# Performance work log

Measured on AMD Instinct MI355X. Metric: run time of the kernel, lower is better.

Reference implementation:

```python
import jax, jax.numpy as jnp
import numpy as np
from jax import lax

# sym8 analysis low-pass filter (pywt.Wavelet('sym8').dec_lo, matches MATLAB Lo_D)
FL = 16
DEC_LO = np.array([-0.0033824159510061256, -0.0005421323317911481, 0.03169508781149298,
                   0.007607487324917605, -0.1432942383508097, -0.061273359067658524,
                   0.4813596512583722, 0.7771857517005235, 0.3644418948353314,
                   -0.051945838107709037, -0.027219029917056003, 0.049137179673607506,
                   0.003808752013890615, -0.01495225833704823, -0.0003029205147213668,
                   0.0018899503327594609])
REC_LO = DEC_LO[::-1]
REC_HI = ((-1.0) ** np.arange(FL)) * DEC_LO  # qmf: rec_hi[k] = (-1)^k * rec_lo[FL-1-k]
DEC_HI = REC_HI[::-1]
# lax.conv does correlation, np.convolve flips -> store flipped filters
_DEC_K = jnp.asarray(np.stack([DEC_LO[::-1], DEC_HI[::-1]])[:, None, :], dtype=jnp.float32)  # (2,1,16)
_REC_K = jnp.asarray(np.stack([REC_LO[::-1], REC_HI[::-1]])[None, :, :], dtype=jnp.float32)  # (1,2,16)
DN = ('NCH', 'OIH', 'NCH')


def _dwt(x):
    # single-level pywt dwt, mode='symmetric': pad FL-1 each side, full conv, take odd indices
    B, C, S = x.shape
    xe = jnp.pad(x.reshape(B * C, 1, S), ((0, 0), (0, 0), (FL - 1, FL - 1)), mode='symmetric')[..., 1:]
    y = lax.conv_general_dilated(xe, _DEC_K, (2,), 'VALID', dimension_numbers=DN)
    L = y.shape[-1]  # floor((S + FL - 1)/2)
    y = y.reshape(B, C, 2, L)
    return y[:, :, 0], y[:, :, 1]


def _idwt(a, d):
    # single-level pywt idwt: upsample (len 2L-1), full conv, trim FL-2 each side
    B, C, L = a.shape
    c = jnp.stack([a, d], axis=2).reshape(B * C, 2, L)
    y = lax.conv_general_dilated(c, _REC_K, (1,), [(1, 1)], lhs_dilation=(2,), dimension_numbers=DN)
    return y.reshape(B, C, y.shape[-1])  # length 2L - FL + 2


def _wavedec(x, level):
    ds = []
    a = x
    for _ in range(level):
        a, d = _dwt(a)
        ds.append(d)
    return a, ds[::-1]  # coarsest first, matching pywt [cA_n, cD_n, ..., cD_1]


def _waverec(a, ds):
    for d in ds:
        if a.shape[-1] == d.shape[-1] + 1:  # static shapes -> Python if is jit-safe
            a = a[..., :-1]
        a = _idwt(a, d)
    return a


def _c1(x, w, b):
    # 1x1 conv: w (O,C), x (B,C,L)
    return jnp.einsum('oc,bcl->bol', w, x) + b[:, None]


def _inorm(x, eps=1e-5):
    m = jnp.mean(x, axis=-1, keepdims=True)
    v = jnp.mean((x - m) ** 2, axis=-1, keepdims=True)
    return (x - m) * lax.rsqrt(v + eps)


def _block(x, w_w, w_b, ca_w, ca_b, cd_w, cd_b, m1_w, m1_b, m2_w, m2_b):
    xn = _inorm(x)
    xs = lax.conv_general_dilated(xn, w_w, (1,), [(1, 1)], dimension_numbers=DN) + w_b[:, None]
    level = cd_w.shape[0]
    a, ds = _wavedec(xn, level)
    a = _c1(a, ca_w, ca_b)
    ds = [_c1(d, cd_w[i], cd_b[i]) for i, d in enumerate(ds)]
    xw = _waverec(a, ds)[..., : xs.shape[-1]]
    xo = x + jax.nn.gelu(xw + xs, approximate=False)
    xon = _inorm(xo)
    h = jax.nn.gelu(_c1(xon, m1_w, m1_b), approximate=False)
    return xo + _c1(h, m2_w, m2_b)


def _forward(x, lift_w, lift_b, blk_w_w, blk_w_b, blk_ca_w, blk_ca_b, blk_cd_w, blk_cd_b,
             blk_m1_w, blk_m1_b, blk_m2_w, blk_m2_b, p1_w, p1_b, p2_w, p2_b):
    B, S = x.shape
    grid = jnp.broadcast_to(jnp.linspace(-1.0, 1.0, S, dtype=x.dtype)[None, None, :], (B, 1, S))
    h = jnp.concatenate([x[:, None, :], grid], axis=1)  # (B, 2, S)
    h = _c1(h, lift_w, lift_b)
    for i in range(blk_w_w.shape[0]):
        h = _block(h, blk_w_w[i], blk_w_b[i], blk_ca_w[i], blk_ca_b[i], blk_cd_w[i],
                   blk_cd_b[i], blk_m1_w[i], blk_m1_b[i], blk_m2_w[i], blk_m2_b[i])
    h = jax.nn.gelu(_c1(h, p1_w, p1_b), approximate=False)
    return _c1(h, p2_w, p2_b)


def setup_inputs():
    key = jax.random.key(0)
    ks = jax.random.split(key, 17)
    B, S, C, NB, LV = 16, 8192, 64, 4, 4
    H = 2 * C  # mlp_expansion=2
    f = jnp.float32
    rn = lambda k, shape, s: jax.random.normal(k, shape, dtype=f) * s
    return {
        'x': jax.random.normal(ks[0], (B, S), dtype=f),
        'lift_w': rn(ks[1], (C, 2), 0.5), 'lift_b': rn(ks[2], (C,), 0.05),
        'blk_w_w': rn(ks[3], (NB, C, C, 3), 0.07), 'blk_w_b': rn(ks[4], (NB, C), 0.05),
        'blk_ca_w': rn(ks[5], (NB, C, C), 0.12), 'blk_ca_b': rn(ks[6], (NB, C), 0.05),
        'blk_cd_w': rn(ks[7], (NB, LV, C, C), 0.12), 'blk_cd_b': rn(ks[8], (NB, LV, C), 0.05),
        'blk_m1_w': rn(ks[9], (NB, H, C), 0.12), 'blk_m1_b': rn(ks[10], (NB, H), 0.05),
        'blk_m2_w': rn(ks[11], (NB, C, H), 0.08), 'blk_m2_b': rn(ks[12], (NB, C), 0.05),
        'p1_w': rn(ks[13], (C // 2, C), 0.12), 'p1_b': rn(ks[14], (C // 2,), 0.05),
        'p2_w': rn(ks[15], (C, C // 2), 0.17), 'p2_b': rn(ks[16], (C,), 0.05),
    }


def reference(x, lift_w, lift_b, blk_w_w, blk_w_b, blk_ca_w, blk_ca_b, blk_cd_w, blk_cd_b,
              blk_m1_w, blk_m1_b, blk_m2_w, blk_m2_b, p1_w, p1_b, p2_w, p2_b):
    return _forward(x, lift_w, lift_b, blk_w_w, blk_w_b, blk_ca_w, blk_ca_b, blk_cd_w,
                    blk_cd_b, blk_m1_w, blk_m1_b, blk_m2_w, blk_m2_b, p1_w, p1_b, p2_w, p2_b)
```

## Files before the change

### kernel.cpp

```cpp
#include <hip/hip_runtime.h>
#include <math.h>

#define S_LEN 8192
#define B_N   16
#define NBC   1024
#define L1v 4103
#define L2v 2059
#define L3v 1037
#define L4v 526
#define LP1 4104
#define LP2 2060
#define LP3 1040
#define LP4 528

#define OFF_CONV 0
#define OFF_M1   49152
#define OFF_M2   81920
#define OFF_CD   114688
#define OFF_CA   180224
#define OFF_P1   196608
#define OFF_P2   198656
#define WTOT     200704

typedef __attribute__((ext_vector_type(8))) short bf16x8;
typedef __attribute__((ext_vector_type(4))) float f32x4;

__constant__ float c_dlo[16] = {
    -0.0033824159510061256f, -0.0005421323317911481f,  0.03169508781149298f,
     0.007607487324917605f,  -0.1432942383508097f,    -0.061273359067658524f,
     0.4813596512583722f,     0.7771857517005235f,     0.3644418948353314f,
    -0.05194583810770904f,   -0.027219029917056003f,   0.049137179673607506f,
     0.003808752013890615f,  -0.01495225833704823f,   -0.0003029205147213668f,
     0.0018899503327594609f
};
__constant__ float c_dhi[16] = {
    -0.0018899503327594609f, -0.0003029205147213668f,  0.01495225833704823f,
     0.003808752013890615f,  -0.049137179673607506f,  -0.027219029917056003f,
     0.05194583810770904f,    0.3644418948353314f,    -0.7771857517005235f,
     0.4813596512583722f,     0.061273359067658524f,  -0.1432942383508097f,
    -0.007607487324917605f,   0.03169508781149298f,    0.0005421323317911481f,
    -0.0033824159510061256f
};

__device__ __forceinline__ float gelu1(float x) {
    return 0.5f * x * (1.0f + erff(x * 0.70710678118654752f));
}
__device__ __forceinline__ float4 load4g(const float* __restrict__ row, int l, int L) {
    float4 v;
    if (l >= 0 && l + 3 < L) {
        v = *(const float4*)(row + l);
    } else {
        v.x = (l     >= 0 && l     < L) ? row[l]     : 0.f;
        v.y = (l + 1 >= 0 && l + 1 < L) ? row[l + 1] : 0.f;
        v.z = (l + 2 >= 0 && l + 2 < L) ? row[l + 2] : 0.f;
        v.w = (l + 3 >= 0 && l + 3 < L) ? row[l + 3] : 0.f;
    }
    return v;
}
__device__ __forceinline__ void store4g(float* __restrict__ row, int l, int L, float4 v) {
    if (l + 3 < L) {
        *(float4*)(row + l) = v;
    } else {
        if (l     < L) row[l]     = v.x;
        if (l + 1 < L) row[l + 1] = v.y;
        if (l + 2 < L) row[l + 2] = v.z;
        if (l + 3 < L) row[l + 3] = v.w;
    }
}
__device__ __forceinline__ ushort f2bf(float f) {
    uint u = __float_as_uint(f);
    u += 0x7fffu + ((u >> 16) & 1u);
    return (ushort)(u >> 16);
}
__device__ __forceinline__ uint pack2bf(float a, float b) {
    return (uint)f2bf(a) | ((uint)f2bf(b) << 16);
}

__global__ __launch_bounds__(256) void prep_kernel(const float* __restrict__ convW,
                                                   const float* __restrict__ m1,
                                                   const float* __restrict__ m2,
                                                   const float* __restrict__ cd,
                                                   const float* __restrict__ ca,
                                                   const float* __restrict__ p1,
                                                   const float* __restrict__ p2,
                                                   ushort* __restrict__ wbuf) {
    int idx = blockIdx.x * 256 + threadIdx.x;
    if (idx >= WTOT) return;
    float v;
    if (idx < OFF_M1) {
        int i = idx / 12288, r = idx % 12288;
        int o = r / 192, k = r % 192;
        int tap = k >> 6, c = k & 63;
        v = convW[i * 12288 + o * 192 + c * 3 + tap];
    } else if (idx < OFF_M2) v = m1[idx - OFF_M1];
    else if (idx < OFF_CD)   v = m2[idx - OFF_M2];
    else if (idx < OFF_CA)   v = cd[idx - OFF_CD];
    else if (idx < OFF_P1)   v = ca[idx - OFF_CA];
    else if (idx < OFF_P2)   v = p1[idx - OFF_P1];
    else                     v = p2[idx - OFF_P2];
    wbuf[idx] = f2bf(v);
}

__global__ __launch_bounds__(256) void lift_kernel(const float* __restrict__ x,
                                                   const float* __restrict__ w,
                                                   const float* __restrict__ bias,
                                                   float* __restrict__ out) {
    int idx = blockIdx.x * 256 + threadIdx.x;
    int s = idx & (S_LEN - 1);
    int r = idx >> 13;
    int o = r & 63;
    int b = r >> 6;
    float g = -1.0f + 2.0f * (float)s / (float)(S_LEN - 1);
    out[idx] = fmaf(w[o * 2 + 0], x[b * S_LEN + s], fmaf(w[o * 2 + 1], g, bias[o]));
}

__global__ __launch_bounds__(256) void stats_kernel(const float* __restrict__ in,
                                                    float2* __restrict__ stats) {
    const int base = blockIdx.x * S_LEN;
    const int tid = threadIdx.x;
    float s = 0.f, ss = 0.f;
#pragma unroll
    for (int i = 0; i < 8; ++i) {
        float4 v = *(const float4*)(in + base + (tid + i * 256) * 4);
        s += v.x + v.y + v.z + v.w;
        ss = fmaf(v.x, v.x, fmaf(v.y, v.y, fmaf(v.z, v.z, fmaf(v.w, v.w, ss))));
    }
    for (int off = 32; off > 0; off >>= 1) {
        s  += __shfl_down(s, off, 64);
        ss += __shfl_down(ss, off, 64);
    }
    __shared__ float sh[8];
    int lane = tid & 63, wv = tid >> 6;
    if (lane == 0) { sh[wv] = s; sh[4 + wv] = ss; }
    __syncthreads();
    if (tid == 0) {
        float tot  = sh[0] + sh[1] + sh[2] + sh[3];
        float tot2 = sh[4] + sh[5] + sh[6] + sh[7];
        float mean = tot * (1.0f / S_LEN);
        float var  = tot2 * (1.0f / S_LEN) - mean * mean;
        stats[blockIdx.x] = make_float2(mean, rsqrtf(var + 1e-5f));
    }
}

#define CWP 200
#define CXP 72

__global__ __launch_bounds__(256) void conv3_mfma_kernel(const float* __restrict__ in,
                                                         float* __restrict__ out,
                                                         const ushort* __restrict__ Wbf,
                                                         const float* __restrict__ bias,
                                                         const float2* __restrict__ stats) {
    __shared__ ushort sW[64 * CWP];
    __shared__ ushort sXt[144 * CXP];
    const int b = blockIdx.y;
    const int n0 = blockIdx.x * 128;
    const int tid = threadIdx.x;

    {
        const int o = tid >> 2, q = tid & 3;
        const uint4* src = (const uint4*)(Wbf + o * 192 + q * 48);
        uint4* dst = (uint4*)(sW + o * CWP + q * 48);
#pragma unroll
        for (int i = 0; i < 6; ++i) dst[i] = src[i];
    }
    {
        const int ch = tid >> 2, q = tid & 3;
        const int rowi = b * 64 + ch;
        const float2 st = stats[rowi];
        const float* row = in + (size_t)rowi * S_LEN;
#pragma unroll
        for (int i = 0; i < 9; ++i) {
            int p = q * 36 + i * 4;
            int l = n0 - 8 + p;
            float4 v;
            if (l >= 0 && l + 3 < S_LEN) {
                v = *(const float4*)(row + l);
                v.x = (v.x - st.x) * st.y; v.y = (v.y - st.x) * st.y;
                v.z = (v.z - st.x) * st.y; v.w = (v.w - st.x) * st.y;
            } else {
                v.x = (l     >= 0 && l     < S_LEN) ? (row[l]     - st.x) * st.y : 0.f;
                v.y = (l + 1 >= 0 && l + 1 < S_LEN) ? (row[l + 1] - st.x) * st.y : 0.f;
                v.z = (l + 2 >= 0 && l + 2 < S_LEN) ? (row[l + 2] - st.x) * st.y : 0.f;
                v.w = (l + 3 >= 0 && l + 3 < S_LEN) ? (row[l + 3] - st.x) * st.y : 0.f;
            }
            sXt[(p + 0) * CXP + ch] = f2bf(v.x);
            sXt[(p + 1) * CXP + ch] = f2bf(v.y);
            sXt[(p + 2) * CXP + ch] = f2bf(v.z);
            sXt[(p + 3) * CXP + ch] = f2bf(v.w);
        }
    }
    __syncthreads();

    const int w = tid >> 6, l = tid & 63, g = l >> 4, c = l & 15;
    f32x4 acc[2][4];
#pragma unroll
    for (int mt = 0; mt < 4; ++mt) {
        float4 bv = *(const float4*)(bias + 16 * mt + 4 * g);
#pragma unroll
        for (int t = 0; t < 2; ++t) {
            acc[t][mt][0] = bv.x; acc[t][mt][1] = bv.y;
            acc[t][mt][2] = bv.z; acc[t][mt][3] = bv.w;
        }
    }
#pragma unroll
    for (int kk = 0; kk < 6; ++kk) {
        const int tap = kk >> 1;
        bf16x8 af[4];
#pragma unroll
        for (int mt = 0; mt < 4; ++mt)
            af[mt] = *(bf16x8*)(sW + (16 * mt + c) * CWP + kk * 32 + 8 * g);
#pragma unroll
        for (int t = 0; t < 2; ++t) {
            const int nl = 32 * w + 16 * t + c;
            const int p = nl + tap + 7;
            bf16x8 xb = *(bf16x8*)(sXt + p * CXP + (kk & 1) * 32 + 8 * g);
#pragma unroll
            for (int mt = 0; mt < 4; ++mt)
                acc[t][mt] = __builtin_amdgcn_mfma_f32_16x16x32_bf16(af[mt], xb, acc[t][mt], 0, 0, 0);
        }
    }
#pragma unroll
    for (int t = 0; t < 2; ++t) {
        const int nl = 32 * w + 16 * t + c;
#pragma unroll
        for (int mt = 0; mt < 4; ++mt)
#pragma unroll
            for (int r = 0; r < 4; ++r) {
                int m = 16 * mt + 4 * g + r;
                out[((size_t)(b * 64 + m)) * S_LEN + n0 + nl] = acc[t][mt][r];
            }
    }
}

#define WMP 72
#define WXP 136

__global__ __launch_bounds__(256) void wmix_kernel(float* __restrict__ d1,
                                                   float* __restrict__ d2,
                                                   float* __restrict__ d3,
                                                   float* __restrict__ d4,
                                                   float* __restrict__ a4,
                                                   const ushort* __restrict__ cdbf,
                                                   const float* __restrict__ cd_b,
                                                   const ushort* __restrict__ cabf,
                                                   const float* __restrict__ ca_b) {
    __shared__ ushort sW[64 * WMP];
    __shared__ ushort sX[64 * WXP];
    const int b = blockIdx.y;
    const int t = blockIdx.x;
    float* buf; const ushort* W; const float* bias; int L, LP, l0;
    if (t < 33)      { buf = d1; W = cdbf + 3 * 4096; bias = cd_b + 3 * 64; L = L1v; LP = LP1; l0 = t * 128; }
    else if (t < 50) { buf = d2; W = cdbf + 2 * 4096; bias = cd_b + 2 * 64; L = L2v; LP = LP2; l0 = (t - 33) * 128; }
    else if (t < 59) { buf = d3; W = cdbf + 1 * 4096; bias = cd_b + 1 * 64; L = L3v; LP = LP3; l0 = (t - 50) * 128; }
    else if (t < 64) { buf = d4; W = cdbf;            bias = cd_b;          L = L4v; LP = LP4; l0 = (t - 59) * 128; }
    else             { buf = a4; W = cabf;            bias = ca_b;          L = L4v; LP = LP4; l0 = (t - 64) * 128; }
    const int tid = threadIdx.x;
    {
        int row = tid >> 2, q = tid & 3;
        const uint4* src = (const uint4*)(W + row * 64 + q * 16);
        uint4* dst = (uint4*)(sW + row * WMP + q * 16);
        dst[0] = src[0]; dst[1] = src[1];
    }
    {
        int ch = tid >> 2, part = tid & 3;
        const float* src = buf + ((size_t)(b * 64 + ch)) * LP;
        uint* dst = (uint*)(sX + ch * WXP + part * 32);
#pragma unroll
        for (int i = 0; i < 8; ++i) {
            int l = l0 + part * 32 + 4 * i;
            float4 v = load4g(src, l, L);
            dst[2 * i]     = pack2bf(v.x, v.y);
            dst[2 * i + 1] = pack2bf(v.z, v.w);
        }
    }
    __syncthreads();
    const int w = tid >> 6, l = tid & 63, g = l >> 4, c = l & 15;
    f32x4 acc[2][4];
#pragma unroll
    for (int mt = 0; mt < 4; ++mt) {
        float4 bv = *(const float4*)(bias + 16 * mt + 4 * g);
#pragma unroll
        for (int tt = 0; tt < 2; ++tt) {
            acc[tt][mt][0] = bv.x; acc[tt][mt][1] = bv.y;
            acc[tt][mt][2] = bv.z; acc[tt][mt][3] = bv.w;
        }
    }
#pragma unroll
    for (int kk = 0; kk < 2; ++kk) {
        bf16x8 af[4];
#pragma unroll
        for (int mt = 0; mt < 4; ++mt)
            af[mt] = *(bf16x8*)(sW + (16 * mt + c) * WMP + kk * 32 + 8 * g);
#pragma unroll
        for (int tt = 0; tt < 2; ++tt) {
            const int nl = 32 * w + 16 * tt + c;
            bf16x8 xb;
#pragma unroll
            for (int j = 0; j < 8; ++j)
                xb[j] = (short)sX[(kk * 32 + 8 * g + j) * WXP + nl];
#pragma unroll
            for (int mt = 0; mt < 4; ++mt)
                acc[tt][mt] = __builtin_amdgcn_mfma_f32_16x16x32_bf16(af[mt], xb, acc[tt][mt], 0, 0, 0);
        }
    }
#pragma unroll
    for (int tt = 0; tt < 2; ++tt) {
        const int nl = 32 * w + 16 * tt + c;
        if (l0 + nl < L) {
#pragma unroll
            for (int mt = 0; mt < 4; ++mt)
#pragma unroll
                for (int r = 0; r < 4; ++r) {
                    int m = 16 * mt + 4 * g + r;
                    buf[((size_t)(b * 64 + m)) * LP + l0 + nl] = acc[tt][mt][r];
                }
        }
    }
}

#define XP2 132
#define MP2 136

__global__ __launch_bounds__(256) void mlp_kernel(float* __restrict__ A,
                                                  const float2* __restrict__ stats,
                                                  const ushort* __restrict__ W1bf,
                                                  const float* __restrict__ b1,
                                                  const ushort* __restrict__ W2bf,
                                                  const float* __restrict__ b2) {
    __shared__ ushort sX [64 * XP2];
    __shared__ ushort sMid[128 * MP2];
    const int b  = blockIdx.y;
    const int n0 = blockIdx.x * 128;
    const int tid = threadIdx.x;

    {
        int ch = tid >> 2, part = tid & 3;
        float2 st = stats[b * 64 + ch];
        const float* src = A + ((size_t)(b * 64 + ch)) * S_LEN + n0 + part * 32;
        uint* dst = (uint*)(sX + ch * XP2 + part * 32);
#pragma unroll
        for (int i = 0; i < 8; ++i) {
            float4 v = *(const float4*)(src + 4 * i);
            v.x = (v.x - st.x) * st.y; v.y = (v.y - st.x) * st.y;
            v.z = (v.z - st.x) * st.y; v.w = (v.w - st.x) * st.y;
            dst[2 * i]     = pack2bf(v.x, v.y);
            dst[2 * i + 1] = pack2bf(v.z, v.w);
        }
    }
    __syncthreads();

    const int w = tid >> 6, l = tid & 63, g = l >> 4, c = l & 15;

#pragma unroll
    for (int tt = 0; tt < 2; ++tt) {
        const int nl = 32 * w + 16 * tt + c;
        bf16x8 xb[2];
#pragma unroll
        for (int kk = 0; kk < 2; ++kk)
#pragma unroll
            for (int j = 0; j < 8; ++j)
                xb[kk][j] = (short)sX[(kk * 32 + 8 * g + j) * XP2 + nl];
        f32x4 acc1[8];
#pragma unroll
        for (int mt = 0; mt < 8; ++mt) {
            float4 bv = *(const float4*)(b1 + 16 * mt + 4 * g);
            acc1[mt][0] = bv.x; acc1[mt][1] = bv.y; acc1[mt][2] = bv.z; acc1[mt][3] = bv.w;
        }
#pragma unroll
        for (int kk = 0; kk < 2; ++kk)
#pragma unroll
            for (int mt = 0; mt < 8; ++mt) {
                bf16x8 af = *(const bf16x8*)(W1bf + (16 * mt + c) * 64 + kk * 32 + 8 * g);
                acc1[mt] = __builtin_amdgcn_mfma_f32_16x16x32_bf16(af, xb[kk], acc1[mt], 0, 0, 0);
            }
#pragma unroll
        for (int mt = 0; mt < 8; ++mt) {
            uint* mp = (uint*)(sMid + nl * MP2 + 16 * mt + 4 * g);
            mp[0] = pack2bf(gelu1(acc1[mt][0]), gelu1(acc1[mt][1]));
            mp[1] = pack2bf(gelu1(acc1[mt][2]), gelu1(acc1[mt][3]));
        }
    }

#pragma unroll
    for (int tt = 0; tt < 2; ++tt) {
        const int nl = 32 * w + 16 * tt + c;
        bf16x8 mb[4];
#pragma unroll
        for (int kk = 0; kk < 4; ++kk)
            mb[kk] = *(bf16x8*)(sMid + nl * MP2 + kk * 32 + 8 * g);
        f32x4 acc2[4];
#pragma unroll
        for (int mt = 0; mt < 4; ++mt) {
            float4 bv = *(const float4*)(b2 + 16 * mt + 4 * g);
            acc2[mt][0] = bv.x; acc2[mt][1] = bv.y; acc2[mt][2] = bv.z; acc2[mt][3] = bv.w;
        }
#pragma unroll
        for (int kk = 0; kk < 4; ++kk)
#pragma unroll
            for (int mt = 0; mt < 4; ++mt) {
                bf16x8 af = *(const bf16x8*)(W2bf + (16 * mt + c) * 128 + kk * 32 + 8 * g);
                acc2[mt] = __builtin_amdgcn_mfma_f32_16x16x32_bf16(af, mb[kk], acc2[mt], 0, 0, 0);
            }
#pragma unroll
        for (int mt = 0; mt < 4; ++mt)
#pragma unroll
            for (int r = 0; r < 4; ++r) {
                int m = 16 * mt + 4 * g + r;
                float* p = A + ((size_t)(b * 64 + m)) * S_LEN + n0 + nl;
                *p = acc2[mt][r] + *p;
            }
    }
}

#define HXP 66
#define HMP 40

__global__ __launch_bounds__(256) void head_kernel(const float* __restrict__ A,
                                                   float* __restrict__ out,
                                                   const ushort* __restrict__ W1bf,
                                                   const float* __restrict__ b1,
                                                   const ushort* __restrict__ W2bf,
                                                   const float* __restrict__ b2) {
    __shared__ ushort sW1[32 * 72];
    __shared__ ushort sW2[64 * HMP];
    __shared__ ushort sX [64 * HXP];
    __shared__ ushort sMid[64 * HMP];
    const int b = blockIdx.y, n0 = blockIdx.x * 64, tid = threadIdx.x;
    {
        int row = tid >> 3, q = tid & 7;
        *(uint4*)(sW1 + row * 72 + q * 8) = *(const uint4*)(W1bf + row * 64 + q * 8);
    }
    {
        int row = tid >> 2, q = tid & 3;
        *(uint4*)(sW2 + row * HMP + q * 8) = *(const uint4*)(W2bf + row * 32 + q * 8);
    }
    {
        int ch = tid >> 2, part = tid & 3;
        const float* src = A + ((size_t)(b * 64 + ch)) * S_LEN + n0 + part * 16;
        uint* dst = (uint*)(sX + ch * HXP + part * 16);
#pragma unroll
        for (int i = 0; i < 4; ++i) {
            float4 v = *(const float4*)(src + 4 * i);
            dst[2 * i] = pack2bf(v.x, v.y); dst[2 * i + 1] = pack2bf(v.z, v.w);
        }
    }
    __syncthreads();
    const int w = tid >> 6, l = tid & 63, g = l >> 4, c = l & 15;
    const int nl = 16 * w + c;
    bf16x8 xb[2];
#pragma unroll
    for (int kk = 0; kk < 2; ++kk)
#pragma unroll
        for (int j = 0; j < 8; ++j)
            xb[kk][j] = (short)sX[(kk * 32 + 8 * g + j) * HXP + nl];
    f32x4 acc1[2];
#pragma unroll
    for (int mt = 0; mt < 2; ++mt) {
        float4 bv = *(const float4*)(b1 + 16 * mt + 4 * g);
        acc1[mt][0] = bv.x; acc1[mt][1] = bv.y; acc1[mt][2] = bv.z; acc1[mt][3] = bv.w;
    }
#pragma unroll
    for (int kk = 0; kk < 2; ++kk)
#pragma unroll
        for (int mt = 0; mt < 2; ++mt) {
            bf16x8 af = *(bf16x8*)(sW1 + (16 * mt + c) * 72 + kk * 32 + 8 * g);
            acc1[mt] = __builtin_amdgcn_mfma_f32_16x16x32_bf16(af, xb[kk], acc1[mt], 0, 0, 0);
        }
#pragma unroll
    for (int mt = 0; mt < 2; ++mt)
#pragma unroll
        for (int r = 0; r < 4; ++r)
            sMid[nl * HMP + 16 * mt + 4 * g + r] = f2bf(gelu1(acc1[mt][r]));
    bf16x8 mb = *(bf16x8*)(sMid + nl * HMP + 8 * g);
    f32x4 acc2[4];
#pragma unroll
    for (int mt = 0; mt < 4; ++mt) {
        float4 bv = *(const float4*)(b2 + 16 * mt + 4 * g);
        acc2[mt][0] = bv.x; acc2[mt][1] = bv.y; acc2[mt][2] = bv.z; acc2[mt][3] = bv.w;
    }
#pragma unroll
    for (int mt = 0; mt < 4; ++mt) {
        bf16x8 af = *(bf16x8*)(sW2 + (16 * mt + c) * HMP + 8 * g);
        acc2[mt] = __builtin_amdgcn_mfma_f32_16x16x32_bf16(af, mb, acc2[mt], 0, 0, 0);
    }
#pragma unroll
    for (int mt = 0; mt < 4; ++mt)
#pragma unroll
        for (int r = 0; r < 4; ++r) {
            int m = 16 * mt + 4 * g + r;
            out[((size_t)(b * 64 + m)) * S_LEN + n0 + nl] = acc2[mt][r];
        }
}

__device__ __forceinline__ void dwt8_core(const float* __restrict__ xb,
                                          float* __restrict__ lo, float* __restrict__ hi) {
#pragma unroll
    for (int j = 0; j < 8; ++j) {
        float l0 = 0.f, h0 = 0.f;
#pragma unroll
        for (int k = 0; k < 16; ++k) {
            float v = xb[2 * j + k + 2];
            l0 = fmaf(v, c_dlo[15 - k], l0);
            h0 = fmaf(v, c_dhi[15 - k], h0);
        }
        lo[j] = l0; hi[j] = h0;
    }
}

__device__ __forceinline__ void dwt_lds_v2(const float* __restrict__ in, int Sin,
                                           float* __restrict__ aout,
                                           float* __restrict__ dout_g, int Lout, int tid) {
    const int NT = (Lout + 7) >> 3;
    for (int g = tid; g < NT; g += 256) {
        float xb[32];
        const int base = 16 * g - 16;
        if (base >= 0 && base + 32 <= Sin) {
#pragma unroll
            for (int q = 0; q < 8; ++q)
                *(float4*)(xb + 4 * q) = *(const float4*)(in + base + 4 * q);
        } else {
#pragma unroll
            for (int loc = 0; loc < 32; ++loc) {
                int i = base + loc;
                i = (i < 0) ? (-1 - i) : i;
                i = (i >= Sin) ? (2 * Sin - 1 - i) : i;
                xb[loc] = in[i];
            }
        }
        float lo[8], hi[8];
        dwt8_core(xb, lo, hi);
        const int t0 = 8 * g;
        if (t0 + 8 <= Lout) {
            *(float4*)(aout + t0)     = make_float4(lo[0], lo[1], lo[2], lo[3]);
            *(float4*)(aout + t0 + 4) = make_float4(lo[4], lo[5], lo[6], lo[7]);
        } else {
#pragma unroll
            for (int j = 0; j < 8; ++j) if (t0 + j < Lout) aout[t0 + j] = lo[j];
        }
        store4g(dout_g, t0,     Lout, make_float4(hi[0], hi[1], hi[2], hi[3]));
        store4g(dout_g, t0 + 4, Lout, make_float4(hi[4], hi[5], hi[6], hi[7]));
    }
}

__global__ __launch_bounds__(256) void dwt_full_kernel(const float* __restrict__ A,
                                                       const float2* __restrict__ stats,
                                                       float* __restrict__ d1,
                                                       float* __restrict__ d2,
                                                       float* __restrict__ d3,
                                                       float* __restrict__ d4,
                                                       float* __restrict__ a4) {
    __shared__ float bufA[4104];
    __shared__ float bufB[2060];
    const int row = blockIdx.x;
    const int tid = threadIdx.x;
    const float2 st = stats[row];
    const float* x = A + (size_t)row * S_LEN;
    float* d1r = d1 + (size_t)row * LP1;

    for (int g = tid; g < 513; g += 256) {
        const int base = 16 * g - 16;
        float xb[32];
        if (base >= 0 && base + 32 <= S_LEN) {
#pragma unroll
            for (int q = 0; q < 8; ++q) {
                float4 v = *(const float4*)(x + base + 4 * q);
                v.x = (v.x - st.x) * st.y; v.y = (v.y - st.x) * st.y;
                v.z = (v.z - st.x) * st.y; v.w = (v.w - st.x) * st.y;
                *(float4*)(xb + 4 * q) = v;
            }
        } else {
#pragma unroll
            for (int loc = 0; loc < 32; ++loc) {
                int i = base + loc;
                i = (i < 0) ? (-1 - i) : i;
                i = (i >= S_LEN) ? (2 * S_LEN - 1 - i) : i;
                xb[loc] = (x[i] - st.x) * st.y;
            }
        }
        float lo[8], hi[8];
        dwt8_core(xb, lo, hi);
        const int t0 = 8 * g;
#pragma unroll
        for (int j = 0; j < 8; ++j)
            if (t0 + j < L1v) bufA[t0 + j] = lo[j];
        store4g(d1r, t0,     L1v, make_float4(hi[0], hi[1], hi[2], hi[3]));
        store4g(d1r, t0 + 4, L1v, make_float4(hi[4], hi[5], hi[6], hi[7]));
    }
    __syncthreads();
    dwt_lds_v2(bufA, L1v, bufB, d2 + (size_t)row * LP2, L2v, tid);
    __syncthreads();
    dwt_lds_v2(bufB, L2v, bufA, d3 + (size_t)row * LP3, L3v, tid);
    __syncthreads();
    dwt_lds_v2(bufA, L3v, bufB, d4 + (size_t)row * LP4, L4v, tid);
    __syncthreads();
    float* a4r = a4 + (size_t)row * LP4;
    for (int i = tid; i < 132; i += 256)
        *(float4*)(a4r + 4 * i) = *(const float4*)(bufB + 4 * i);
}

__device__ __forceinline__ void idwt8_regs(const float* __restrict__ a,
                                           const float* __restrict__ d,
                                           int g, int Lc, float* __restrict__ y) {
    float av[12], dv[12];
    const int m0 = 4 * g;
    if (m0 + 12 <= Lc) {
#pragma unroll
        for (int q = 0; q < 3; ++q) {
            *(float4*)(av + 4 * q) = *(const float4*)(a + m0 + 4 * q);
            *(float4*)(dv + 4 * q) = *(const float4*)(d + m0 + 4 * q);
        }
    } else {
#pragma unroll
        for (int jj = 0; jj < 12; ++jj) {
            int m = m0 + jj;
            bool ok = (m < Lc);
            av[jj] = ok ? a[m] : 0.f;
            dv[jj] = ok ? d[m] : 0.f;
        }
    }
#pragma unroll
    for (int e = 0; e < 4; ++e) {
        float ye = 0.f, yo = 0.f;
#pragma unroll
        for (int j = 0; j < 8; ++j) {
            ye = fmaf(av[e + j], c_dlo[2 * j + 1], ye);
            ye = fmaf(dv[e + j], c_dlo[14 - 2 * j], ye);
            yo = fmaf(av[e + j], c_dlo[2 * j], yo);
            yo = fmaf(dv[e + j], -c_dlo[15 - 2 * j], yo);
        }
        y[2 * e] = ye;
        y[2 * e + 1] = yo;
    }
}

__device__ __forceinline__ void idwt_lds_v2(const float* __restrict__ a,
                                            const float* __restrict__ d,
                                            int Lc, int Lout, float* __restrict__ out, int tid) {
    const int NT = (Lout + 7) >> 3;
    for (int g = tid; g < NT; g += 256) {
        float y[8];
        idwt8_regs(a, d, g, Lc, y);
        const int t0 = 8 * g;
        if (t0 + 8 <= Lout) {
            *(float4*)(out + t0)     = make_float4(y[0], y[1], y[2], y[3]);
            *(float4*)(out + t0 + 4) = make_float4(y[4], y[5], y[6], y[7]);
        } else {
#pragma unroll
            for (int j = 0; j < 8; ++j) if (t0 + j < Lout) out[t0 + j] = y[j];
        }
    }
}

__device__ __forceinline__ void gload_lds(const float* __restrict__ src, int Lv,
                                          float* __restrict__ dst, int tid) {
    const int NG = (Lv + 3) >> 2;
    for (int i = tid; i < NG; i += 256)
        *(float4*)(dst + 4 * i) = load4g(src, 4 * i, Lv);
}

__global__ __launch_bounds__(256) void idwt_full_kernel(const float* __restrict__ a4,
                                                        const float* __restrict__ d4,
                                                        const float* __restrict__ d3,
                                                        const float* __restrict__ d2,
                                                        const float* __restrict__ d1,
                                                        float* __restrict__ h,
                                                        const float* __restrict__ xs,
                                                        float2* __restrict__ statsOut) {
    __shared__ float bufY[4104];
    __shared__ float bufA[4104];
    __shared__ float bufD[4104];
    const int row = blockIdx.x;
    const int tid = threadIdx.x;

    gload_lds(a4 + (size_t)row * LP4, L4v, bufA, tid);
    gload_lds(d4 + (size_t)row * LP4, L4v, bufD, tid);
    __syncthreads();
    idwt_lds_v2(bufA, bufD, L4v, 1038, bufY, tid);
    __syncthreads();
    gload_lds(d3 + (size_t)row * LP3, L3v, bufD, tid);
    __syncthreads();
    idwt_lds_v2(bufY, bufD, L3v, 2060, bufA, tid);
    __syncthreads();
    gload_lds(d2 + (size_t)row * LP2, L2v, bufD, tid);
    __syncthreads();
    idwt_lds_v2(bufA, bufD, L2v, 4104, bufY, tid);
    __syncthreads();
    gload_lds(d1 + (size_t)row * LP1, L1v, bufD, tid);
    __syncthreads();

    float* hrow = h + (size_t)row * S_LEN;
    const float* srow = xs + (size_t)row * S_LEN;
    float s = 0.f, ss = 0.f;
#pragma unroll
    for (int it = 0; it < 4; ++it) {
        const int g = it * 256 + tid;
        float y[8];
        idwt8_regs(bufY, bufD, g, L1v, y);
        const int t0 = 8 * g;
#pragma unroll
        for (int q = 0; q < 2; ++q) {
            float4 sv = *(const float4*)(srow + t0 + 4 * q);
            float4 hv = *(const float4*)(hrow + t0 + 4 * q);
            hv.x += gelu1(y[4 * q + 0] + sv.x);
            hv.y += gelu1(y[4 * q + 1] + sv.y);
            hv.z += gelu1(y[4 * q + 2] + sv.z);
            hv.w += gelu1(y[4 * q + 3] + sv.w);
            *(float4*)(hrow + t0 + 4 * q) = hv;
            s += hv.x + hv.y + hv.z + hv.w;
            ss = fmaf(hv.x, hv.x, fmaf(hv.y, hv.y, fmaf(hv.z, hv.z, fmaf(hv.w, hv.w, ss))));
        }
    }
    for (int off = 32; off > 0; off >>= 1) {
        s  += __shfl_down(s, off, 64);
        ss += __shfl_down(ss, off, 64);
    }
    __syncthreads();
    int lane = tid & 63, wv = tid >> 6;
    if (lane == 0) { bufA[wv] = s; bufA[4 + wv] = ss; }
    __syncthreads();
    if (tid == 0) {
        float tot  = bufA[0] + bufA[1] + bufA[2] + bufA[3];
        float tot2 = bufA[4] + bufA[5] + bufA[6] + bufA[7];
        float mean = tot * (1.0f / S_LEN);
        float var  = tot2 * (1.0f / S_LEN) - mean * mean;
        statsOut[row] = make_float2(mean, rsqrtf(var + 1e-5f));
    }
}

extern "C" void kernel_launch(void* const* d_in, const int* in_sizes, int n_in,
                              void* d_out, int out_size, void* d_ws, size_t ws_size,
                              hipStream_t stream) {
    const float* x       = (const float*)d_in[0];
    const float* lift_w  = (const float*)d_in[1];
    const float* lift_b  = (const float*)d_in[2];
    const float* blk_w_w = (const float*)d_in[3];
    const float* blk_w_b = (const float*)d_in[4];
    const float* blk_ca_w= (const float*)d_in[5];
    const float* blk_ca_b= (const float*)d_in[6];
    const float* blk_cd_w= (const float*)d_in[7];
    const float* blk_cd_b= (const float*)d_in[8];
    const float* blk_m1_w= (const float*)d_in[9];
    const float* blk_m1_b= (const float*)d_in[10];
    const float* blk_m2_w= (const float*)d_in[11];
    const float* blk_m2_b= (const float*)d_in[12];
    const float* p1_w    = (const float*)d_in[13];
    const float* p1_b    = (const float*)d_in[14];
    const float* p2_w    = (const float*)d_in[15];
    const float* p2_b    = (const float*)d_in[16];

    float* ws = (float*)d_ws;
    const size_t T32 = (size_t)NBC * S_LEN;
    float* A  = ws;
    float* Cc = ws + 2 * T32;
    float* d1 = ws + 4 * T32;
    float* d2 = d1 + (size_t)NBC * LP1;
    float* d3 = d2 + (size_t)NBC * LP2;
    float* d4 = d3 + (size_t)NBC * LP3;
    float* ap0 = d4 + (size_t)NBC * LP4;
    float* ap1 = ap0 + (size_t)NBC * 4104;
    float2* statsBuf = (float2*)(ap1 + (size_t)NBC * 4104);
    ushort* wbuf = (ushort*)(statsBuf + NBC);

    dim3 blk(256);

    prep_kernel<<<(WTOT + 255) / 256, blk, 0, stream>>>(blk_w_w, blk_m1_w, blk_m2_w,
                                                        blk_cd_w, blk_ca_w, p1_w, p2_w, wbuf);
    lift_kernel<<<(NBC * S_LEN) / 256, blk, 0, stream>>>(x, lift_w, lift_b, A);

    for (int i = 0; i < 4; ++i) {
        const float* w_b  = blk_w_b  + (size_t)i * 64;
        const float* ca_b = blk_ca_b + (size_t)i * 64;
        const float* cd_b = blk_cd_b + (size_t)i * 4 * 64;
        const float* m1_b = blk_m1_b + (size_t)i * 128;
        const float* m2_b = blk_m2_b + (size_t)i * 64;
        const ushort* convbf = wbuf + OFF_CONV + (size_t)i * 12288;
        const ushort* m1bf   = wbuf + OFF_M1   + (size_t)i * 8192;
        const ushort* m2bf   = wbuf + OFF_M2   + (size_t)i * 8192;
        const ushort* cdbf   = wbuf + OFF_CD   + (size_t)i * 16384;
        const ushort* cabf   = wbuf + OFF_CA   + (size_t)i * 4096;

        stats_kernel<<<NBC, blk, 0, stream>>>(A, statsBuf);
        conv3_mfma_kernel<<<dim3(S_LEN / 128, B_N), blk, 0, stream>>>(A, Cc, convbf, w_b, statsBuf);
        dwt_full_kernel<<<NBC, blk, 0, stream>>>(A, statsBuf, d1, d2, d3, d4, ap1);

        wmix_kernel<<<dim3(69, B_N), blk, 0, stream>>>(d1, d2, d3, d4, ap1,
                                                       cdbf, cd_b, cabf, ca_b);

        idwt_full_kernel<<<NBC, blk, 0, stream>>>(ap1, d4, d3, d2, d1, A, Cc, statsBuf);
        mlp_kernel<<<dim3(S_LEN / 128, B_N), blk, 0, stream>>>(A, statsBuf, m1bf, m1_b, m2bf, m2_b);
    }

    head_kernel<<<dim3(S_LEN / 64, B_N), blk, 0, stream>>>(A, (float*)d_out,
                                                           wbuf + OFF_P1, p1_b,
                                                           wbuf + OFF_P2, p2_b);
}
```

Baseline: 839.3 us.

## Store intermediate wavelet and conv buffers in bf16; stage MLP weights in LDS

The conv3 output and the DWT detail and approximation buffers are now written and read as bf16 instead of fp32. This halves global traffic between the conv, dwt, wmix and idwt kernels and lets wmix copy bf16 directly into shared memory without converting. The MLP kernel now loads its two weight matrices into LDS, processes 64-column tiles with more blocks, and loops over a single tile per wave. The cost is extra rounding of the intermediates and more LDS use per MLP block.

Result: faster. 682.0 us (-18.7%).

```diff
diff --git a/kernel.cpp b/kernel.cpp
--- a/kernel.cpp
+++ b/kernel.cpp
@@ -8,10 +8,10 @@
 #define L2v 2059
 #define L3v 1037
 #define L4v 526
-#define LP1 4104
-#define LP2 2060
-#define LP3 1040
-#define LP4 528
+#define LB1 4104
+#define LB2 2064
+#define LB3 1040
+#define LB4 528
 
 #define OFF_CONV 0
 #define OFF_M1   49152
@@ -57,16 +57,6 @@
     }
     return v;
 }
-__device__ __forceinline__ void store4g(float* __restrict__ row, int l, int L, float4 v) {
-    if (l + 3 < L) {
-        *(float4*)(row + l) = v;
-    } else {
-        if (l     < L) row[l]     = v.x;
-        if (l + 1 < L) row[l + 1] = v.y;
-        if (l + 2 < L) row[l + 2] = v.z;
-        if (l + 3 < L) row[l + 3] = v.w;
-    }
-}
 __device__ __forceinline__ ushort f2bf(float f) {
     uint u = __float_as_uint(f);
     u += 0x7fffu + ((u >> 16) & 1u);
@@ -74,6 +64,9 @@
 }
 __device__ __forceinline__ uint pack2bf(float a, float b) {
     return (uint)f2bf(a) | ((uint)f2bf(b) << 16);
+}
+__device__ __forceinline__ float bfu(ushort u) {
+    return __uint_as_float(((uint)u) << 16);
 }
 
 __global__ __launch_bounds__(256) void prep_kernel(const float* __restrict__ convW,
@@ -146,7 +139,7 @@
 #define CXP 72
 
 __global__ __launch_bounds__(256) void conv3_mfma_kernel(const float* __restrict__ in,
-                                                         float* __restrict__ out,
+                                                         ushort* __restrict__ out,
                                                          const ushort* __restrict__ Wbf,
                                                          const float* __restrict__ bias,
                                                          const float2* __restrict__ stats) {
@@ -227,7 +220,7 @@
 #pragma unroll
             for (int r = 0; r < 4; ++r) {
                 int m = 16 * mt + 4 * g + r;
-                out[((size_t)(b * 64 + m)) * S_LEN + n0 + nl] = acc[t][mt][r];
+                out[((size_t)(b * 64 + m)) * S_LEN + n0 + nl] = f2bf(acc[t][mt][r]);
             }
     }
 }
@@ -235,11 +228,11 @@
 #define WMP 72
 #define WXP 136
 
-__global__ __launch_bounds__(256) void wmix_kernel(float* __restrict__ d1,
-                                                   float* __restrict__ d2,
-                                                   float* __restrict__ d3,
-                                                   float* __restrict__ d4,
-                                                   float* __restrict__ a4,
+__global__ __launch_bounds__(256) void wmix_kernel(ushort* __restrict__ d1,
+                                                   ushort* __restrict__ d2,
+                                                   ushort* __restrict__ d3,
+                                                   ushort* __restrict__ d4,
+                                                   ushort* __restrict__ a4,
                                                    const ushort* __restrict__ cdbf,
                                                    const float* __restrict__ cd_b,
                                                    const ushort* __restrict__ cabf,
@@ -248,12 +241,12 @@
     __shared__ ushort sX[64 * WXP];
     const int b = blockIdx.y;
     const int t = blockIdx.x;
-    float* buf; const ushort* W; const float* bias; int L, LP, l0;
-    if (t < 33)      { buf = d1; W = cdbf + 3 * 4096; bias = cd_b + 3 * 64; L = L1v; LP = LP1; l0 = t * 128; }
-    else if (t < 50) { buf = d2; W = cdbf + 2 * 4096; bias = cd_b + 2 * 64; L = L2v; LP = LP2; l0 = (t - 33) * 128; }
-    else if (t < 59) { buf = d3; W = cdbf + 1 * 4096; bias = cd_b + 1 * 64; L = L3v; LP = LP3; l0 = (t - 50) * 128; }
-    else if (t < 64) { buf = d4; W = cdbf;            bias = cd_b;          L = L4v; LP = LP4; l0 = (t - 59) * 128; }
-    else             { buf = a4; W = cabf;            bias = ca_b;          L = L4v; LP = LP4; l0 = (t - 64) * 128; }
+    ushort* buf; const ushort* W; const float* bias; int L, LP, l0;
+    if (t < 33)      { buf = d1; W = cdbf + 3 * 4096; bias = cd_b + 3 * 64; L = L1v; LP = LB1; l0 = t * 128; }
+    else if (t < 50) { buf = d2; W = cdbf + 2 * 4096; bias = cd_b + 2 * 64; L = L2v; LP = LB2; l0 = (t - 33) * 128; }
+    else if (t < 59) { buf = d3; W = cdbf + 1 * 4096; bias = cd_b + 1 * 64; L = L3v; LP = LB3; l0 = (t - 50) * 128; }
+    else if (t < 64) { buf = d4; W = cdbf;            bias = cd_b;          L = L4v; LP = LB4; l0 = (t - 59) * 128; }
+    else             { buf = a4; W = cabf;            bias = ca_b;          L = L4v; LP = LB4; l0 = (t - 64) * 128; }
     const int tid = threadIdx.x;
     {
         int row = tid >> 2, q = tid & 3;
@@ -263,14 +256,18 @@
     }
     {
         int ch = tid >> 2, part = tid & 3;
-        const float* src = buf + ((size_t)(b * 64 + ch)) * LP;
-        uint* dst = (uint*)(sX + ch * WXP + part * 32);
-#pragma unroll
-        for (int i = 0; i < 8; ++i) {
-            int l = l0 + part * 32 + 4 * i;
-            float4 v = load4g(src, l, L);
-            dst[2 * i]     = pack2bf(v.x, v.y);
-            dst[2 * i + 1] = pack2bf(v.z, v.w);
+        const ushort* src = buf + ((size_t)(b * 64 + ch)) * LP;
+#pragma unroll
+        for (int i = 0; i < 4; ++i) {
+            int l = l0 + part * 32 + 8 * i;
+            ushort* dst = sX + ch * WXP + part * 32 + 8 * i;
+            if (l + 8 <= L) {
+                *(uint4*)dst = *(const uint4*)(src + l);
+            } else {
+#pragma unroll
+                for (int j = 0; j < 8; ++j)
+                    dst[j] = (l + j < L) ? src[l + j] : (ushort)0;
+            }
         }
     }
     __syncthreads();
@@ -312,14 +309,16 @@
 #pragma unroll
                 for (int r = 0; r < 4; ++r) {
                     int m = 16 * mt + 4 * g + r;
-                    buf[((size_t)(b * 64 + m)) * LP + l0 + nl] = acc[tt][mt][r];
+                    buf[((size_t)(b * 64 + m)) * LP + l0 + nl] = f2bf(acc[tt][mt][r]);
                 }
         }
     }
 }
 
-#define XP2 132
-#define MP2 136
+#define W1P 72
+#define W2P 136
+#define XP  66
+#define MP  136
 
 __global__ __launch_bounds__(256) void mlp_kernel(float* __restrict__ A,
                                                   const float2* __restrict__ stats,
@@ -327,19 +326,35 @@
                                                   const float* __restrict__ b1,
                                                   const ushort* __restrict__ W2bf,
                                                   const float* __restrict__ b2) {
-    __shared__ ushort sX [64 * XP2];
-    __shared__ ushort sMid[128 * MP2];
+    __shared__ ushort sW1[128 * W1P];
+    __shared__ ushort sW2[64 * W2P];
+    __shared__ ushort sX [64 * XP];
+    __shared__ ushort sMid[64 * MP];
     const int b  = blockIdx.y;
-    const int n0 = blockIdx.x * 128;
+    const int n0 = blockIdx.x * 64;
     const int tid = threadIdx.x;
 
+    {
+#pragma unroll
+        for (int e = tid; e < 1024; e += 256) {
+            int row = e >> 3, q = e & 7;
+            *(uint4*)(sW1 + row * W1P + q * 8) = *(const uint4*)(W1bf + row * 64 + q * 8);
+        }
+    }
+    {
+#pragma unroll
+        for (int e = tid; e < 1024; e += 256) {
+            int row = e >> 4, q = e & 15;
+            *(uint4*)(sW2 + row * W2P + q * 8) = *(const uint4*)(W2bf + row * 128 + q * 8);
+        }
+    }
     {
         int ch = tid >> 2, part = tid & 3;
         float2 st = stats[b * 64 + ch];
-        const float* src = A + ((size_t)(b * 64 + ch)) * S_LEN + n0 + part * 32;
-        uint* dst = (uint*)(sX + ch * XP2 + part * 32);
-#pragma unroll
-        for (int i = 0; i < 8; ++i) {
+        const float* src = A + ((size_t)(b * 64 + ch)) * S_LEN + n0 + part * 16;
+        uint* dst = (uint*)(sX + ch * XP + part * 16);
+#pragma unroll
+        for (int i = 0; i < 4; ++i) {
             float4 v = *(const float4*)(src + 4 * i);
             v.x = (v.x - st.x) * st.y; v.y = (v.y - st.x) * st.y;
             v.z = (v.z - st.x) * st.y; v.w = (v.w - st.x) * st.y;
@@ -349,66 +364,67 @@
     }
     __syncthreads();
 
-    const int w = tid >> 6, l = tid & 63, g = l >> 4, c = l & 15;
-
-#pragma unroll
-    for (int tt = 0; tt < 2; ++tt) {
-        const int nl = 32 * w + 16 * tt + c;
-        bf16x8 xb[2];
-#pragma unroll
-        for (int kk = 0; kk < 2; ++kk)
-#pragma unroll
-            for (int j = 0; j < 8; ++j)
-                xb[kk][j] = (short)sX[(kk * 32 + 8 * g + j) * XP2 + nl];
-        f32x4 acc1[8];
+    const int w = tid >> 6;
+    const int l = tid & 63;
+    const int g = l >> 4;
+    const int c = l & 15;
+    const int nl = 16 * w + c;
+
+    bf16x8 xb[2];
+#pragma unroll
+    for (int kk = 0; kk < 2; ++kk)
+#pragma unroll
+        for (int j = 0; j < 8; ++j)
+            xb[kk][j] = (short)sX[(kk * 32 + 8 * g + j) * XP + nl];
+
+    f32x4 acc1[8];
+#pragma unroll
+    for (int mt = 0; mt < 8; ++mt) {
+        float4 bv = *(const float4*)(b1 + 16 * mt + 4 * g);
+        acc1[mt][0] = bv.x; acc1[mt][1] = bv.y; acc1[mt][2] = bv.z; acc1[mt][3] = bv.w;
+    }
+#pragma unroll
+    for (int kk = 0; kk < 2; ++kk) {
 #pragma unroll
         for (int mt = 0; mt < 8; ++mt) {
-            float4 bv = *(const float4*)(b1 + 16 * mt + 4 * g);
-            acc1[mt][0] = bv.x; acc1[mt][1] = bv.y; acc1[mt][2] = bv.z; acc1[mt][3] = bv.w;
-        }
-#pragma unroll
-        for (int kk = 0; kk < 2; ++kk)
-#pragma unroll
-            for (int mt = 0; mt < 8; ++mt) {
-                bf16x8 af = *(const bf16x8*)(W1bf + (16 * mt + c) * 64 + kk * 32 + 8 * g);
-                acc1[mt] = __builtin_amdgcn_mfma_f32_16x16x32_bf16(af, xb[kk], acc1[mt], 0, 0, 0);
-            }
-#pragma unroll
-        for (int mt = 0; mt < 8; ++mt) {
-            uint* mp = (uint*)(sMid + nl * MP2 + 16 * mt + 4 * g);
-            mp[0] = pack2bf(gelu1(acc1[mt][0]), gelu1(acc1[mt][1]));
-            mp[1] = pack2bf(gelu1(acc1[mt][2]), gelu1(acc1[mt][3]));
-        }
-    }
-
-#pragma unroll
-    for (int tt = 0; tt < 2; ++tt) {
-        const int nl = 32 * w + 16 * tt + c;
-        bf16x8 mb[4];
-#pragma unroll
-        for (int kk = 0; kk < 4; ++kk)
-            mb[kk] = *(bf16x8*)(sMid + nl * MP2 + kk * 32 + 8 * g);
-        f32x4 acc2[4];
+            bf16x8 af = *(bf16x8*)(sW1 + (16 * mt + c) * W1P + kk * 32 + 8 * g);
+            acc1[mt] = __builtin_amdgcn_mfma_f32_16x16x32_bf16(af, xb[kk], acc1[mt], 0, 0, 0);
+        }
+    }
+#pragma unroll
+    for (int mt = 0; mt < 8; ++mt) {
+        uint* mp = (uint*)(sMid + nl * MP + 16 * mt + 4 * g);
+        mp[0] = pack2bf(gelu1(acc1[mt][0]), gelu1(acc1[mt][1]));
+        mp[1] = pack2bf(gelu1(acc1[mt][2]), gelu1(acc1[mt][3]));
+    }
+
+    bf16x8 mb[4];
+#pragma unroll
+    for (int kk = 0; kk < 4; ++kk)
+        mb[kk] = *(bf16x8*)(sMid + nl * MP + kk * 32 + 8 * g);
+
+    f32x4 acc2[4];
+#pragma unroll
+    for (int mt = 0; mt < 4; ++mt) {
+        float4 bv = *(const float4*)(b2 + 16 * mt + 4 * g);
+        acc2[mt][0] = bv.x; acc2[mt][1] = bv.y; acc2[mt][2] = bv.z; acc2[mt][3] = bv.w;
+    }
+#pragma unroll
+    for (int kk = 0; kk < 4; ++kk) {
 #pragma unroll
         for (int mt = 0; mt < 4; ++mt) {
-            float4 bv = *(const float4*)(b2 + 16 * mt + 4 * g);
-            acc2[mt][0] = bv.x; acc2[mt][1] = bv.y; acc2[mt][2] = bv.z; acc2[mt][3] = bv.w;
-        }
-#pragma unroll
-        for (int kk = 0; kk < 4; ++kk)
-#pragma unroll
-            for (int mt = 0; mt < 4; ++mt) {
-                bf16x8 af = *(const bf16x8*)(W2bf + (16 * mt + c) * 128 + kk * 32 + 8 * g);
-                acc2[mt] = __builtin_amdgcn_mfma_f32_16x16x32_bf16(af, mb[kk], acc2[mt], 0, 0, 0);
-            }
-#pragma unroll
-        for (int mt = 0; mt < 4; ++mt)
-#pragma unroll
-            for (int r = 0; r < 4; ++r) {
-                int m = 16 * mt + 4 * g + r;
-                float* p = A + ((size_t)(b * 64 + m)) * S_LEN + n0 + nl;
-                *p = acc2[mt][r] + *p;
-            }
+            bf16x8 af = *(bf16x8*)(sW2 + (16 * mt + c) * W2P + kk * 32 + 8 * g);
+            acc2[mt] = __builtin_amdgcn_mfma_f32_16x16x32_bf16(af, mb[kk], acc2[mt], 0, 0, 0);
+        }
+    }
+#pragma unroll
+    for (int mt = 0; mt < 4; ++mt) {
+#pragma unroll
+        for (int r = 0; r < 4; ++r) {
+            int m = 16 * mt + 4 * g + r;
+            float* p = A + ((size_t)(b * 64 + m)) * S_LEN + n0 + nl;
+            *p = acc2[mt][r] + *p;
+        }
     }
 }
 
@@ -507,9 +523,23 @@
     }
 }
 
+__device__ __forceinline__ void store_bf8(ushort* __restrict__ dst, int t0, int Lout,
+                                          const float* __restrict__ v) {
+    if (t0 + 8 <= Lout) {
+        uint4 u;
+        u.x = pack2bf(v[0], v[1]); u.y = pack2bf(v[2], v[3]);
+        u.z = pack2bf(v[4], v[5]); u.w = pack2bf(v[6], v[7]);
+        *(uint4*)(dst + t0) = u;
+    } else {
+#pragma unroll
+        for (int j = 0; j < 8; ++j)
+            if (t0 + j < Lout) dst[t0 + j] = f2bf(v[j]);
+    }
+}
+
 __device__ __forceinline__ void dwt_lds_v2(const float* __restrict__ in, int Sin,
                                            float* __restrict__ aout,
-                                           float* __restrict__ dout_g, int Lout, int tid) {
+                                           ushort* __restrict__ dout_g, int Lout, int tid) {
     const int NT = (Lout + 7) >> 3;
     for (int g = tid; g < NT; g += 256) {
         float xb[32];
@@ -537,25 +567,24 @@
 #pragma unroll
             for (int j = 0; j < 8; ++j) if (t0 + j < Lout) aout[t0 + j] = lo[j];
         }
-        store4g(dout_g, t0,     Lout, make_float4(hi[0], hi[1], hi[2], hi[3]));
-        store4g(dout_g, t0 + 4, Lout, make_float4(hi[4], hi[5], hi[6], hi[7]));
+        store_bf8(dout_g, t0, Lout, hi);
     }
 }
 
 __global__ __launch_bounds__(256) void dwt_full_kernel(const float* __restrict__ A,
                                                        const float2* __restrict__ stats,
-                                                       float* __restrict__ d1,
-                                                       float* __restrict__ d2,
-                                                       float* __restrict__ d3,
-                                                       float* __restrict__ d4,
-                                                       float* __restrict__ a4) {
+                                                       ushort* __restrict__ d1,
+                                                       ushort* __restrict__ d2,
+                                                       ushort* __restrict__ d3,
+                                                       ushort* __restrict__ d4,
+                                                       ushort* __restrict__ a4) {
     __shared__ float bufA[4104];
-    __shared__ float bufB[2060];
+    __shared__ float bufB[2064];
     const int row = blockIdx.x;
     const int tid = threadIdx.x;
     const float2 st = stats[row];
     const float* x = A + (size_t)row * S_LEN;
-    float* d1r = d1 + (size_t)row * LP1;
+    ushort* d1r = d1 + (size_t)row * LB1;
 
     for (int g = tid; g < 513; g += 256) {
         const int base = 16 * g - 16;
@@ -583,19 +612,24 @@
 #pragma unroll
         for (int j = 0; j < 8; ++j)
             if (t0 + j < L1v) bufA[t0 + j] = lo[j];
-        store4g(d1r, t0,     L1v, make_float4(hi[0], hi[1], hi[2], hi[3]));
-        store4g(d1r, t0 + 4, L1v, make_float4(hi[4], hi[5], hi[6], hi[7]));
-    }
-    __syncthreads();
-    dwt_lds_v2(bufA, L1v, bufB, d2 + (size_t)row * LP2, L2v, tid);
-    __syncthreads();
-    dwt_lds_v2(bufB, L2v, bufA, d3 + (size_t)row * LP3, L3v, tid);
-    __syncthreads();
-    dwt_lds_v2(bufA, L3v, bufB, d4 + (size_t)row * LP4, L4v, tid);
-    __syncthreads();
-    float* a4r = a4 + (size_t)row * LP4;
-    for (int i = tid; i < 132; i += 256)
-        *(float4*)(a4r + 4 * i) = *(const float4*)(bufB + 4 * i);
+        store_bf8(d1r, t0, L1v, hi);
+    }
+    __syncthreads();
+    dwt_lds_v2(bufA, L1v, bufB, d2 + (size_t)row * LB2, L2v, tid);
+    __syncthreads();
+    dwt_lds_v2(bufB, L2v, bufA, d3 + (size_t)row * LB3, L3v, tid);
+    __syncthreads();
+    dwt_lds_v2(bufA, L3v, bufB, d4 + (size_t)row * LB4, L4v, tid);
+    __syncthreads();
+    ushort* a4r = a4 + (size_t)row * LB4;
+    for (int g = tid; g < 66; g += 256) {
+        const int t0 = 8 * g;
+        float v[8];
+#pragma unroll
+        for (int j = 0; j < 8; ++j)
+            v[j] = (t0 + j < L4v) ? bufB[t0 + j] : 0.f;
+        store_bf8(a4r, t0, 528, v);
+    }
 }
 
 __device__ __forceinline__ void idwt8_regs(const float* __restrict__ a,
@@ -651,20 +685,30 @@
     }
 }
 
-__device__ __forceinline__ void gload_lds(const float* __restrict__ src, int Lv,
-                                          float* __restrict__ dst, int tid) {
-    const int NG = (Lv + 3) >> 2;
-    for (int i = tid; i < NG; i += 256)
-        *(float4*)(dst + 4 * i) = load4g(src, 4 * i, Lv);
-}
-
-__global__ __launch_bounds__(256) void idwt_full_kernel(const float* __restrict__ a4,
-                                                        const float* __restrict__ d4,
-                                                        const float* __restrict__ d3,
-                                                        const float* __restrict__ d2,
-                                                        const float* __restrict__ d1,
+__device__ __forceinline__ void gload_lds_bf(const ushort* __restrict__ src, int Lv,
+                                             float* __restrict__ dst, int tid) {
+    const int NG = (Lv + 7) >> 3;
+    for (int g = tid; g < NG; g += 256) {
+        uint4 u = *(const uint4*)(src + 8 * g);
+        float v[8];
+        v[0] = bfu((ushort)u.x); v[1] = bfu((ushort)(u.x >> 16));
+        v[2] = bfu((ushort)u.y); v[3] = bfu((ushort)(u.y >> 16));
+        v[4] = bfu((ushort)u.z); v[5] = bfu((ushort)(u.z >> 16));
+        v[6] = bfu((ushort)u.w); v[7] = bfu((ushort)(u.w >> 16));
+        const int t0 = 8 * g;
+#pragma unroll
+        for (int j = 0; j < 8; ++j)
+            dst[t0 + j] = (t0 + j < Lv) ? v[j] : 0.f;
+    }
+}
+
+__global__ __launch_bounds__(256) void idwt_full_kernel(const ushort* __restrict__ a4,
+                                                        const ushort* __restrict__ d4,
+                                                        const ushort* __restrict__ d3,
+                                                        const ushort* __restrict__ d2,
+                                                        const ushort* __restrict__ d1,
                                                         float* __restrict__ h,
-                                                        const float* __restrict__ xs,
+                                                        const ushort* __restrict__ xs,
                                                         float2* __restrict__ statsOut) {
     __shared__ float bufY[4104];
     __shared__ float bufA[4104];
@@ -672,24 +716,24 @@
     const int row = blockIdx.x;
     const int tid = threadIdx.x;
 
-    gload_lds(a4 + (size_t)row * LP4, L4v, bufA, tid);
-    gload_lds(d4 + (size_t)row * LP4, L4v, bufD, tid);
+    gload_lds_bf(a4 + (size_t)row * LB4, L4v, bufA, tid);
+    gload_lds_bf(d4 + (size_t)row * LB4, L4v, bufD, tid);
     __syncthreads();
     idwt_lds_v2(bufA, bufD, L4v, 1038, bufY, tid);
     __syncthreads();
-    gload_lds(d3 + (size_t)row * LP3, L3v, bufD, tid);
+    gload_lds_bf(d3 + (size_t)row * LB3, L3v, bufD, tid);
     __syncthreads();
     idwt_lds_v2(bufY, bufD, L3v, 2060, bufA, tid);
     __syncthreads();
-    gload_lds(d2 + (size_t)row * LP2, L2v, bufD, tid);
+    gload_lds_bf(d2 + (size_t)row * LB2, L2v, bufD, tid);
     __syncthreads();
     idwt_lds_v2(bufA, bufD, L2v, 4104, bufY, tid);
     __syncthreads();
-    gload_lds(d1 + (size_t)row * LP1, L1v, bufD, tid);
+    gload_lds_bf(d1 + (size_t)row * LB1, L1v, bufD, tid);
     __syncthreads();
 
     float* hrow = h + (size_t)row * S_LEN;
-    const float* srow = xs + (size_t)row * S_LEN;
+    const ushort* srow = xs + (size_t)row * S_LEN;
     float s = 0.f, ss = 0.f;
 #pragma unroll
     for (int it = 0; it < 4; ++it) {
@@ -699,12 +743,12 @@
         const int t0 = 8 * g;
 #pragma unroll
         for (int q = 0; q < 2; ++q) {
-            float4 sv = *(const float4*)(srow + t0 + 4 * q);
+            uint2 sp = *(const uint2*)(srow + t0 + 4 * q);
             float4 hv = *(const float4*)(hrow + t0 + 4 * q);
-            hv.x += gelu1(y[4 * q + 0] + sv.x);
-            hv.y += gelu1(y[4 * q + 1] + sv.y);
-            hv.z += gelu1(y[4 * q + 2] + sv.z);
-            hv.w += gelu1(y[4 * q + 3] + sv.w);
+            hv.x += gelu1(y[4 * q + 0] + bfu((ushort)sp.x));
+            hv.y += gelu1(y[4 * q + 1] + bfu((ushort)(sp.x >> 16)));
+            hv.z += gelu1(y[4 * q + 2] + bfu((ushort)sp.y));
+            hv.w += gelu1(y[4 * q + 3] + bfu((ushort)(sp.y >> 16)));
             *(float4*)(hrow + t0 + 4 * q) = hv;
             s += hv.x + hv.y + hv.z + hv.w;
             ss = fmaf(hv.x, hv.x, fmaf(hv.y, hv.y, fmaf(hv.z, hv.z, fmaf(hv.w, hv.w, ss))));
@@ -751,14 +795,13 @@
     float* ws = (float*)d_ws;
     const size_t T32 = (size_t)NBC * S_LEN;
     float* A  = ws;
-    float* Cc = ws + 2 * T32;
-    float* d1 = ws + 4 * T32;
-    float* d2 = d1 + (size_t)NBC * LP1;
-    float* d3 = d2 + (size_t)NBC * LP2;
-    float* d4 = d3 + (size_t)NBC * LP3;
-    float* ap0 = d4 + (size_t)NBC * LP4;
-    float* ap1 = ap0 + (size_t)NBC * 4104;
-    float2* statsBuf = (float2*)(ap1 + (size_t)NBC * 4104);
+    ushort* Cc = (ushort*)(ws + T32);
+    ushort* d1 = Cc + T32;
+    ushort* d2 = d1 + (size_t)NBC * LB1;
+    ushort* d3 = d2 + (size_t)NBC * LB2;
+    ushort* d4 = d3 + (size_t)NBC * LB3;
+    ushort* a4 = d4 + (size_t)NBC * LB4;
+    float2* statsBuf = (float2*)(a4 + (size_t)NBC * LB4 + 8);
     ushort* wbuf = (ushort*)(statsBuf + NBC);
 
     dim3 blk(256);
@@ -781,13 +824,13 @@
 
         stats_kernel<<<NBC, blk, 0, stream>>>(A, statsBuf);
         conv3_mfma_kernel<<<dim3(S_LEN / 128, B_N), blk, 0, stream>>>(A, Cc, convbf, w_b, statsBuf);
-        dwt_full_kernel<<<NBC, blk, 0, stream>>>(A, statsBuf, d1, d2, d3, d4, ap1);
-
-        wmix_kernel<<<dim3(69, B_N), blk, 0, stream>>>(d1, d2, d3, d4, ap1,
+        dwt_full_kernel<<<NBC, blk, 0, stream>>>(A, statsBuf, d1, d2, d3, d4, a4);
+
+        wmix_kernel<<<dim3(69, B_N), blk, 0, stream>>>(d1, d2, d3, d4, a4,
                                                        cdbf, cd_b, cabf, ca_b);
 
-        idwt_full_kernel<<<NBC, blk, 0, stream>>>(ap1, d4, d3, d2, d1, A, Cc, statsBuf);
-        mlp_kernel<<<dim3(S_LEN / 128, B_N), blk, 0, stream>>>(A, statsBuf, m1bf, m1_b, m2bf, m2_b);
+        idwt_full_kernel<<<NBC, blk, 0, stream>>>(a4, d4, d3, d2, d1, A, Cc, statsBuf);
+        mlp_kernel<<<dim3(S_LEN / 64, B_N), blk, 0, stream>>>(A, statsBuf, m1bf, m1_b, m2bf, m2_b);
     }
 
     head_kernel<<<dim3(S_LEN / 64, B_N), blk, 0, stream>>>(A, (float*)d_out,
```
